# Kernel optimization log

Hardware: AMD Instinct MI355X
Metric: run time of the kernel (lower is better)

Reference implementation:

```python
import jax, jax.numpy as jnp
import numpy as np

NUM_SELECT = 300
OUT_H = 448
OUT_W = 448


def setup_inputs() -> dict:
    key = jax.random.key(0)
    k1, k2, k3 = jax.random.split(key, 3)
    B, Q, C = 4, 900, 91
    pred_logits = jax.random.normal(k1, (B, Q, C), dtype=jnp.float32)
    pred_boxes = jax.random.uniform(k2, (B, Q, 4), dtype=jnp.float32)  # cxcywh in [0,1)
    pred_masks = jax.random.normal(k3, (B, Q, 28, 28), dtype=jnp.float32)
    # all images same size so resize output shape is static under jit
    target_sizes = jnp.full((B, 2), OUT_H, dtype=jnp.int64 if jax.config.jax_enable_x64 else jnp.int32)
    return {"pred_logits": pred_logits, "pred_boxes": pred_boxes,
            "pred_masks": pred_masks, "target_sizes": target_sizes}


def _box_cxcywh_to_xyxy(b):
    cx, cy, w, h = jnp.split(b, 4, axis=-1)
    return jnp.concatenate([cx - 0.5 * w, cy - 0.5 * h, cx + 0.5 * w, cy + 0.5 * h], axis=-1)


def reference(pred_logits, pred_boxes, pred_masks, target_sizes):
    B, Q, C = pred_logits.shape
    # sigmoid + topk over flattened (query, class) axis
    prob = jax.nn.sigmoid(pred_logits).reshape(B, Q * C)
    scores, topk_idx = jax.lax.top_k(prob, NUM_SELECT)          # [B, K]
    topk_boxes = topk_idx // C                                   # query index [B, K]
    labels = topk_idx % C                                        # class index [B, K]

    boxes = _box_cxcywh_to_xyxy(pred_boxes)                      # [B, Q, 4]
    boxes = jnp.take_along_axis(boxes, topk_boxes[:, :, None], axis=1)  # [B, K, 4]

    img_h = target_sizes[:, 0].astype(boxes.dtype)
    img_w = target_sizes[:, 1].astype(boxes.dtype)
    scale = jnp.stack([img_w, img_h, img_w, img_h], axis=1)      # [B, 4]
    boxes = boxes * scale[:, None, :]

    # gather top-k masks: [B, K, 28, 28]
    masks = jnp.take_along_axis(pred_masks, topk_boxes[:, :, None, None], axis=1)
    masks = masks.astype(jnp.float16)
    # bilinear, half-pixel centers == torch align_corners=False
    resize_one = lambda m: jax.image.resize(m, (NUM_SELECT, OUT_H, OUT_W), method="bilinear")
    masks = jax.vmap(resize_one)(masks)                          # [B, K, OUT_H, OUT_W] fp16

    return scores, labels, boxes, masks
```

## Files before the change

### kernel.cpp

```cpp
#include <hip/hip_runtime.h>
#include <hip/hip_fp16.h>

#define QN 900
#define CN 91
#define TOTN (QN * CN)
#define KSEL 300
#define BN 4
#define OUTW 448
#define MASKPIX (OUTW * OUTW)
#define OFFS_LABELS (BN * KSEL)
#define OFFS_BOXES  (2 * BN * KSEL)
#define OFFS_MASKS  (6 * BN * KSEL)
#define MAXC 1024
#define BT 1024
#define NWAVE (BT / 64)

typedef float floatx4 __attribute__((ext_vector_type(4)));

static __device__ __forceinline__ unsigned fkey(float f) {
    unsigned u = __float_as_uint(f);
    return (u & 0x80000000u) ? ~u : (u | 0x80000000u);
}

__global__ __launch_bounds__(BT) void select_kernel(
    const float* __restrict__ logits, const float* __restrict__ boxes,
    const int* __restrict__ tsz, float* out, int* qsel)
{
    const int b = blockIdx.x;
    const int tid = threadIdx.x;
    const int wid = tid >> 6;
    const float* lg = logits + (size_t)b * TOTN;

    __shared__ unsigned h16[NWAVE][256];
    __shared__ unsigned hist[256];
    __shared__ int sh_bin, sh_want;
    __shared__ unsigned sh_cnt;
    __shared__ int cidx[MAXC];
    __shared__ unsigned ckey[MAXC];

    for (int i = tid; i < NWAVE * 256; i += BT)
        ((unsigned*)h16)[i] = 0;
    __syncthreads();
    for (int i = tid; i < TOTN; i += BT) {
        unsigned key = fkey(lg[i]);
        atomicAdd(&h16[wid][key >> 24], 1u);
    }
    __syncthreads();
    if (tid < 256) {
        unsigned s = 0;
        for (int w = 0; w < NWAVE; ++w) s += h16[w][tid];
        hist[tid] = s;
    }
    __syncthreads();

    unsigned prefix = 0;
    int want = KSEL;
    for (int round = 0; round < 4; ++round) {
        const int shift = 24 - 8 * round;
        if (round > 0) {
            const unsigned pmask = 0xFFFFFFFFu << (shift + 8);
            if (tid < 256) hist[tid] = 0;
            __syncthreads();
            for (int i = tid; i < TOTN; i += BT) {
                unsigned key = fkey(lg[i]);
                if ((key & pmask) == prefix)
                    atomicAdd(&hist[(key >> shift) & 255u], 1u);
            }
            __syncthreads();
        }
        if (tid == 0) {
            int acc = 0;
            int bin = 255;
            for (; bin > 0; --bin) {
                int c = (int)hist[bin];
                if (acc + c >= want) break;
                acc += c;
            }
            sh_bin = bin;
            sh_want = want - acc;
        }
        __syncthreads();
        prefix |= ((unsigned)sh_bin << shift);
        want = sh_want;
        __syncthreads();
    }
    const unsigned T = prefix;

    if (tid == 0) sh_cnt = 0;
    __syncthreads();
    for (int i = tid; i < TOTN; i += BT) {
        unsigned key = fkey(lg[i]);
        if (key >= T) {
            unsigned pos = atomicAdd(&sh_cnt, 1u);
            if (pos < MAXC) { cidx[pos] = i; ckey[pos] = key; }
        }
    }
    __syncthreads();
    const int ncand = min((int)sh_cnt, MAXC);

    const float fh = (float)tsz[b * 2 + 0];
    const float fw = (float)tsz[b * 2 + 1];

    for (int c = tid; c < ncand; c += BT) {
        const unsigned kc = ckey[c];
        const int ic = cidx[c];
        int rank = 0;
        for (int s = 0; s < ncand; ++s) {
            unsigned ks = ckey[s];
            if (ks > kc || (ks == kc && cidx[s] < ic)) ++rank;
        }
        if (rank < KSEL) {
            float lf = lg[ic];
            float score = 1.0f / (1.0f + expf(-lf));
            int q = ic / CN;
            int label = ic - q * CN;

            out[b * KSEL + rank] = score;
            out[OFFS_LABELS + b * KSEL + rank] = (float)label;

            const float* bx = boxes + ((size_t)b * QN + q) * 4;
            float cx = bx[0], cy = bx[1], ww = bx[2], hh = bx[3];
            float* ob = out + OFFS_BOXES + ((size_t)(b * KSEL + rank)) * 4;
            ob[0] = (cx - 0.5f * ww) * fw;
            ob[1] = (cy - 0.5f * hh) * fh;
            ob[2] = (cx + 0.5f * ww) * fw;
            ob[3] = (cy + 0.5f * hh) * fh;

            qsel[b * KSEL + rank] = q;
        }
    }
}

#define SPLIT 4
#define ROWSB (OUTW / SPLIT)

__global__ __launch_bounds__(256) void mask_kernel(
    const float* __restrict__ masks, const int* __restrict__ qsel,
    float* __restrict__ out)
{
    const int mk = blockIdx.x >> 2;
    const int part = blockIdx.x & 3;
    const int b = mk / KSEL;
    const int q = qsel[mk];
    const float* __restrict__ src = masks + ((size_t)b * QN + q) * 784;

    const int j = threadIdx.x & 127;
    const int rhalf = threadIdx.x >> 7;
    if (j >= 112) return;

    const int qd = j & 3;
    const int i4 = j >> 2;
    const int c0 = i4 - 1 + (qd >> 1);
    const int c0c = c0 < 0 ? 0 : c0;
    const int c1c = (c0 + 1 > 27) ? 27 : c0 + 1;
    const float toff = 0.25f * (float)qd - ((qd >= 2) ? 1.0f : 0.0f);
    const float t0 = 0.53125f + toff, t1 = 0.59375f + toff,
                t2 = 0.65625f + toff, t3 = 0.71875f + toff;

    const int ybase = part * ROWSB + rhalf;
    float* optr = out + OFFS_MASKS + (size_t)mk * MASKPIX
                + (size_t)ybase * OUTW + j * 4;

    float sy = (float)ybase * 0.0625f - 0.46875f;
    for (int k = 0; k < ROWSB / 2; ++k) {
        float yf = floorf(sy);
        float ty = sy - yf;
        int iy = (int)yf;
        int y0 = iy < 0 ? 0 : iy;
        int y1 = (iy + 1 > 27) ? 27 : iy + 1;
        const float* r0 = src + y0 * 28;
        const float* r1 = src + y1 * 28;
        float m00 = r0[c0c], m01 = r0[c1c];
        float m10 = r1[c0c], m11 = r1[c1c];
        float v0 = fmaf(ty, m10 - m00, m00);
        float v1 = fmaf(ty, m11 - m01, m01);
        float dv = v1 - v0;
        floatx4 w;
        w.x = fmaf(t0, dv, v0);
        w.y = fmaf(t1, dv, v0);
        w.z = fmaf(t2, dv, v0);
        w.w = fmaf(t3, dv, v0);
        __builtin_nontemporal_store(w, reinterpret_cast<floatx4*>(optr));
        optr += 2 * OUTW;
        sy += 0.125f;
    }
}

extern "C" void kernel_launch(void* const* d_in, const int* in_sizes, int n_in,
                              void* d_out, int out_size, void* d_ws, size_t ws_size,
                              hipStream_t stream) {
    const float* pred_logits = (const float*)d_in[0];
    const float* pred_boxes  = (const float*)d_in[1];
    const float* pred_masks  = (const float*)d_in[2];
    const int*   target_sz   = (const int*)d_in[3];
    float* out = (float*)d_out;
    int* qsel = (int*)d_ws;

    select_kernel<<<BN, BT, 0, stream>>>(pred_logits, pred_boxes, target_sz, out, qsel);
    mask_kernel<<<BN * KSEL * SPLIT, 256, 0, stream>>>(pred_masks, qsel, out);
}
```

Baseline: 310.3 us.

## Cut radix select to two passes, per-lane histograms, parallel bin scan

The radix select now stops after two 8-bit digit passes instead of four, keeping every element whose top 16 bits reach the threshold. The exact order is still settled by the existing rank-counting step over the candidate buffer, which grows from 1024 to 2048 entries. The first histogram uses padded per-lane counters to spread atomic contention, and the serial bin scan becomes a wave-level suffix-sum search. The mask stores switch from nontemporal to regular vector stores. The risk is more candidates, which makes the quadratic ranking step costlier, and possible overflow if more than 2048 share the top 16 bits.

New measurement: 272.6 us. -12.1%, faster.

```diff
diff --git a/kernel.cpp b/kernel.cpp
--- a/kernel.cpp
+++ b/kernel.cpp
@@ -11,9 +11,8 @@
 #define OFFS_LABELS (BN * KSEL)
 #define OFFS_BOXES  (2 * BN * KSEL)
 #define OFFS_MASKS  (6 * BN * KSEL)
-#define MAXC 1024
+#define MAXC 2048
 #define BT 1024
-#define NWAVE (BT / 64)
 
 typedef float floatx4 __attribute__((ext_vector_type(4)));
 
@@ -28,71 +27,89 @@
 {
     const int b = blockIdx.x;
     const int tid = threadIdx.x;
-    const int wid = tid >> 6;
+    const int lane = tid & 63;
     const float* lg = logits + (size_t)b * TOTN;
 
-    __shared__ unsigned h16[NWAVE][256];
+    __shared__ unsigned hlane[256 * 33];
     __shared__ unsigned hist[256];
-    __shared__ int sh_bin, sh_want;
-    __shared__ unsigned sh_cnt;
+    __shared__ int sh_bin, sh_want, sh_chunk;
+    __shared__ unsigned sh_above, sh_cnt;
     __shared__ int cidx[MAXC];
     __shared__ unsigned ckey[MAXC];
 
-    for (int i = tid; i < NWAVE * 256; i += BT)
-        ((unsigned*)h16)[i] = 0;
-    __syncthreads();
-    for (int i = tid; i < TOTN; i += BT) {
-        unsigned key = fkey(lg[i]);
-        atomicAdd(&h16[wid][key >> 24], 1u);
+    for (int i = tid; i < 256 * 33; i += BT) hlane[i] = 0;
+    __syncthreads();
+    {
+        const int sl = lane & 31;
+        for (int i = tid; i < TOTN; i += BT) {
+            unsigned key = fkey(lg[i]);
+            atomicAdd(&hlane[(key >> 24) * 33 + sl], 1u);
+        }
     }
     __syncthreads();
     if (tid < 256) {
         unsigned s = 0;
-        for (int w = 0; w < NWAVE; ++w) s += h16[w][tid];
+#pragma unroll
+        for (int l = 0; l < 32; ++l) s += hlane[tid * 33 + l];
         hist[tid] = s;
     }
     __syncthreads();
 
     unsigned prefix = 0;
     int want = KSEL;
-    for (int round = 0; round < 4; ++round) {
+#pragma unroll
+    for (int round = 0; round < 2; ++round) {
         const int shift = 24 - 8 * round;
         if (round > 0) {
-            const unsigned pmask = 0xFFFFFFFFu << (shift + 8);
             if (tid < 256) hist[tid] = 0;
             __syncthreads();
             for (int i = tid; i < TOTN; i += BT) {
                 unsigned key = fkey(lg[i]);
-                if ((key & pmask) == prefix)
-                    atomicAdd(&hist[(key >> shift) & 255u], 1u);
+                if ((key & 0xFF000000u) == prefix)
+                    atomicAdd(&hist[(key >> 16) & 255u], 1u);
             }
             __syncthreads();
         }
+        if (tid < 64) {
+            unsigned p = hist[tid * 4] + hist[tid * 4 + 1]
+                       + hist[tid * 4 + 2] + hist[tid * 4 + 3];
+            unsigned suffix = p;
+#pragma unroll
+            for (int o = 1; o < 64; o <<= 1) {
+                unsigned t = __shfl_down(suffix, o);
+                if (tid + o < 64) suffix += t;
+            }
+            unsigned nxt = __shfl_down(suffix, 1);
+            if (tid == 63) nxt = 0;
+            bool flag = (suffix >= (unsigned)want) && (nxt < (unsigned)want);
+            if (flag) { sh_chunk = tid; sh_above = nxt; }
+        }
+        __syncthreads();
         if (tid == 0) {
-            int acc = 0;
-            int bin = 255;
-            for (; bin > 0; --bin) {
-                int c = (int)hist[bin];
-                if (acc + c >= want) break;
-                acc += c;
+            int ch = sh_chunk;
+            unsigned acc = sh_above;
+            int j = 3;
+            for (; j > 0; --j) {
+                if (acc + hist[ch * 4 + j] >= (unsigned)want) break;
+                acc += hist[ch * 4 + j];
             }
-            sh_bin = bin;
-            sh_want = want - acc;
+            sh_bin = ch * 4 + j;
+            sh_want = want - (int)acc;
         }
         __syncthreads();
         prefix |= ((unsigned)sh_bin << shift);
         want = sh_want;
         __syncthreads();
     }
-    const unsigned T = prefix;
+    const unsigned T16 = prefix >> 16;
 
     if (tid == 0) sh_cnt = 0;
     __syncthreads();
     for (int i = tid; i < TOTN; i += BT) {
         unsigned key = fkey(lg[i]);
-        if (key >= T) {
-            unsigned pos = atomicAdd(&sh_cnt, 1u);
-            if (pos < MAXC) { cidx[pos] = i; ckey[pos] = key; }
+        if ((key >> 16) >= T16) {
+            unsigned p = atomicAdd(&sh_cnt, 1u);
+            if (p < MAXC) { cidx[p] = i; ckey[p] = key; }
         }
     }
     __syncthreads();
@@ -180,7 +197,7 @@
         w.y = fmaf(t1, dv, v0);
         w.z = fmaf(t2, dv, v0);
         w.w = fmaf(t3, dv, v0);
-        __builtin_nontemporal_store(w, reinterpret_cast<floatx4*>(optr));
+        *reinterpret_cast<floatx4*>(optr) = w;
         optr += 2 * OUTW;
         sy += 0.125f;
     }
```
